# Kernel optimization log

Hardware: AMD Instinct MI355X
Metric: run time of the kernel (lower is better)

The kernel has to match this reference:

```python
import jax, jax.numpy as jnp
import numpy as np

N_PRED = 50000
N_GT = 2000


def _make_boxes(key, n, coord_scale=1000.0, wh_scale=100.0):
    k1, k2 = jax.random.split(key)
    xy = jax.random.uniform(k1, (n, 2), dtype=jnp.float32) * coord_scale
    wh = jax.random.uniform(k2, (n, 2), dtype=jnp.float32) * wh_scale + 1.0
    return jnp.concatenate([xy, xy + wh], axis=-1)  # xyxy


def setup_inputs() -> dict:
    key = jax.random.key(0)
    kp, kg = jax.random.split(key)
    return {
        "pred_bbox": _make_boxes(kp, N_PRED),
        "gt_bbox": _make_boxes(kg, N_GT),
    }


def _bbox_overlap(pred, gt):
    # pred: [N,4], gt: [M,4], xyxy -> IoU matrix [N,M]
    lt = jnp.maximum(pred[:, None, :2], gt[None, :, :2])  # [N,M,2]
    rb = jnp.minimum(pred[:, None, 2:], gt[None, :, 2:])  # [N,M,2]
    wh = jnp.clip(rb - lt, 0.0)
    inter = wh[..., 0] * wh[..., 1]  # [N,M]
    area_p = (pred[:, 2] - pred[:, 0]) * (pred[:, 3] - pred[:, 1])  # [N]
    area_g = (gt[:, 2] - gt[:, 0]) * (gt[:, 3] - gt[:, 1])  # [M]
    union = area_p[:, None] + area_g[None, :] - inter
    return inter / union


def reference(pred_bbox, gt_bbox):
    # OverlapCalculator.calc_overlap: detach pred, pairwise IoU, row-wise max
    iou = _bbox_overlap(jax.lax.stop_gradient(pred_bbox), gt_bbox)  # [N,M]
    max_overlap = jnp.max(iou, axis=1)          # [N]
    argmax_overlap = jnp.argmax(iou, axis=1)    # [N] int
    # forward returns (pred_bbox, gt_bbox, max, argmax) per image pair
    return (pred_bbox, gt_bbox, max_overlap, argmax_overlap)
```

## Files before the change

### kernel.cpp

```cpp
#include <hip/hip_runtime.h>


#define N_PRED 50000
#define N_GT   2000
#define NBIN   512
#define BLOCK  256
#define LPP    8
#define PPB    (BLOCK / LPP)

__device__ __forceinline__ int bin_of(float x, float xmin, float invw) {
    int b = (int)floorf((x - xmin) * invw);
    return max(0, min(NBIN - 1, b));
}

__global__ __launch_bounds__(512) void build_index(
        const float4* __restrict__ gt,
        float4* __restrict__ ws_gt, unsigned short* __restrict__ ws_idx,
        int* __restrict__ ws_bin, float* __restrict__ ws_par,
        float* __restrict__ out) {
#pragma clang fp contract(off)
    __shared__ float rmin[512], rmax[512], rw[512];
    __shared__ int   hist[NBIN], scan[NBIN], cursor[NBIN];
    __shared__ float s_par[3];
    const int tid = threadIdx.x;

    float mn = 3.4e38f, mx = -3.4e38f, mw = 0.0f;
    for (int j = tid; j < N_GT; j += 512) {
        const float4 g = gt[j];
        mn = fminf(mn, g.x);
        mx = fmaxf(mx, g.x);
        mw = fmaxf(mw, g.z - g.x);
        ((float4*)(out + 4 * N_PRED))[j] = g;
    }
    rmin[tid] = mn; rmax[tid] = mx; rw[tid] = mw;
    __syncthreads();
    for (int s = 256; s > 0; s >>= 1) {
        if (tid < s) {
            rmin[tid] = fminf(rmin[tid], rmin[tid + s]);
            rmax[tid] = fmaxf(rmax[tid], rmax[tid + s]);
            rw[tid]   = fmaxf(rw[tid],   rw[tid + s]);
        }
        __syncthreads();
    }
    if (tid == 0) {
        const float xmin  = rmin[0];
        const float range = fmaxf(rmax[0] - xmin, 1e-20f);
        s_par[0] = xmin;
        s_par[1] = (float)NBIN / range;
        s_par[2] = rw[0];
        ws_par[0] = s_par[0]; ws_par[1] = s_par[1]; ws_par[2] = s_par[2];
    }
    hist[tid] = 0;
    __syncthreads();
    const float xmin = s_par[0], invw = s_par[1];

    for (int j = tid; j < N_GT; j += 512)
        atomicAdd(&hist[bin_of(gt[j].x, xmin, invw)], 1);
    __syncthreads();

    const int v = hist[tid];
    scan[tid] = v;
    __syncthreads();
    for (int off = 1; off < NBIN; off <<= 1) {
        const int t = (tid >= off) ? scan[tid - off] : 0;
        __syncthreads();
        scan[tid] += t;
        __syncthreads();
    }
    const int excl = scan[tid] - v;
    cursor[tid] = excl;
    ws_bin[tid] = excl;
    if (tid == NBIN - 1) ws_bin[NBIN] = scan[tid];
    __syncthreads();

    for (int j = tid; j < N_GT; j += 512) {
        const float4 g = gt[j];
        const int pos = atomicAdd(&cursor[bin_of(g.x, xmin, invw)], 1);
        ws_gt[pos]  = g;
        ws_idx[pos] = (unsigned short)j;
    }
}

__global__ __launch_bounds__(BLOCK) void iou_max(
        const float4* __restrict__ pred,
        const float4* __restrict__ ws_gt, const unsigned short* __restrict__ ws_idx,
        const int* __restrict__ ws_bin, const float* __restrict__ ws_par,
        float* __restrict__ out) {
#pragma clang fp contract(off)
    __shared__ float4         sgt[N_GT];
    __shared__ unsigned short sidx[N_GT];
    __shared__ int            sbin[NBIN + 1];

    for (int j = threadIdx.x; j < N_GT; j += BLOCK) {
        sgt[j]  = ws_gt[j];
        sidx[j] = ws_idx[j];
    }
    for (int j = threadIdx.x; j < NBIN + 1; j += BLOCK) sbin[j] = ws_bin[j];
    const float xmin = ws_par[0], invw = ws_par[1], mgw = ws_par[2];
    __syncthreads();

    const int  pid = blockIdx.x * PPB + (int)(threadIdx.x >> 3);
    const int  sub = threadIdx.x & (LPP - 1);
    const bool act = pid < N_PRED;
    const float4 p  = pred[act ? pid : 0];
    const float  ap = (p.z - p.x) * (p.w - p.y);

    int lo = 0, hi = 0;
    if (act) {
        const int bl = bin_of(p.x - mgw - 0.5f, xmin, invw);
        const int bh = bin_of(p.z, xmin, invw);
        lo = sbin[bl];
        hi = sbin[bh + 1];
    }

    float best = 0.0f;
    int   bidx = 0;
    for (int t = lo + sub; t < hi; t += LPP) {
        const float4 g  = sgt[t];
        const int    oi = sidx[t];
        const float  ag = (g.z - g.x) * (g.w - g.y);
        const float  w  = fmaxf(fminf(p.z, g.z) - fmaxf(p.x, g.x), 0.0f);
        const float  h  = fmaxf(fminf(p.w, g.w) - fmaxf(p.y, g.y), 0.0f);
        const float  in = w * h;
        const float  un = (ap + ag) - in;
        const float  q  = in / un;
        if (q > best || (q == best && oi < bidx)) { best = q; bidx = oi; }
    }
#pragma unroll
    for (int s = 1; s < LPP; s <<= 1) {
        const float oq = __shfl_xor(best, s);
        const int   oi = __shfl_xor(bidx, s);
        if (oq > best || (oq == best && oi < bidx)) { best = oq; bidx = oi; }
    }
    if (act && sub == 0) {
        ((float4*)out)[pid] = p;
        out[4 * N_PRED + 4 * N_GT + pid]          = best;
        out[4 * N_PRED + 4 * N_GT + N_PRED + pid] = (float)bidx;
    }
}

extern "C" void kernel_launch(void* const* d_in, const int* in_sizes, int n_in,
                              void* d_out, int out_size, void* d_ws, size_t ws_size,
                              hipStream_t stream) {
    const float4* pred = (const float4*)d_in[0];
    const float4* gt   = (const float4*)d_in[1];
    float* out = (float*)d_out;

    char* ws = (char*)d_ws;
    float4*         ws_gt  = (float4*)ws;
    unsigned short* ws_idx = (unsigned short*)(ws + 32768);
    int*            ws_bin = (int*)(ws + 32768 + 4096);
    float*          ws_par = (float*)(ws + 32768 + 4096 + 2304);

    build_index<<<1, 512, 0, stream>>>(gt, ws_gt, ws_idx, ws_bin, ws_par, out);

    const int gx = (N_PRED + PPB - 1) / PPB;
    iou_max<<<gx, BLOCK, 0, stream>>>(pred, ws_gt, ws_idx, ws_bin, ws_par, out);
}
```

Before: 89.91 us.

## Replace 1D x-bin index with 2D x/y grid for GT candidate pruning

Builds a 32x16 spatial grid over ground-truth boxes (x-major, y-minor cells) instead of 512 x-only bins. Each prediction walks its x-bin range and, per x-bin, scans only the contiguous run of y-cells that could overlap, so far fewer non-overlapping GT boxes get an IoU evaluation. In exchange it adds a per-x-bin outer loop with two shared loads each, and the coarser x bins mean more per-column overhead and shorter inner loops for the 8 lanes to split.

```diff
diff --git a/kernel.cpp b/kernel.cpp
--- a/kernel.cpp
+++ b/kernel.cpp
@@ -3,65 +3,79 @@
 
 #define N_PRED 50000
 #define N_GT   2000
-#define NBIN   512
+#define NXB    32
+#define NYB    16
+#define NCELL  (NXB * NYB)
 #define BLOCK  256
 #define LPP    8
 #define PPB    (BLOCK / LPP)
 
-__device__ __forceinline__ int bin_of(float x, float xmin, float invw) {
-    int b = (int)floorf((x - xmin) * invw);
-    return max(0, min(NBIN - 1, b));
+__device__ __forceinline__ int bin1(float v, float mn, float inv, int nb) {
+    int b = (int)floorf((v - mn) * inv);
+    return max(0, min(nb - 1, b));
 }
 
 __global__ __launch_bounds__(512) void build_index(
         const float4* __restrict__ gt,
         float4* __restrict__ ws_gt, unsigned short* __restrict__ ws_idx,
-        int* __restrict__ ws_bin, float* __restrict__ ws_par,
+        int* __restrict__ ws_cell, float* __restrict__ ws_par,
         float* __restrict__ out) {
 #pragma clang fp contract(off)
-    __shared__ float rmin[512], rmax[512], rw[512];
-    __shared__ int   hist[NBIN], scan[NBIN], cursor[NBIN];
-    __shared__ float s_par[3];
+    __shared__ float rxm[512], rxM[512], rym[512], ryM[512], rw[512], rh[512];
+    __shared__ int   hist[NCELL], scan[NCELL], cursor[NCELL];
+    __shared__ float s_par[6];
     const int tid = threadIdx.x;
 
-    float mn = 3.4e38f, mx = -3.4e38f, mw = 0.0f;
+    float xm = 3.4e38f, xM = -3.4e38f, ym = 3.4e38f, yM = -3.4e38f;
+    float w = 0.0f, h = 0.0f;
     for (int j = tid; j < N_GT; j += 512) {
         const float4 g = gt[j];
-        mn = fminf(mn, g.x);
-        mx = fmaxf(mx, g.x);
-        mw = fmaxf(mw, g.z - g.x);
+        xm = fminf(xm, g.x); xM = fmaxf(xM, g.x);
+        ym = fminf(ym, g.y); yM = fmaxf(yM, g.y);
+        w  = fmaxf(w, g.z - g.x);
+        h  = fmaxf(h, g.w - g.y);
         ((float4*)(out + 4 * N_PRED))[j] = g;
     }
-    rmin[tid] = mn; rmax[tid] = mx; rw[tid] = mw;
+    rxm[tid] = xm; rxM[tid] = xM; rym[tid] = ym; ryM[tid] = yM;
+    rw[tid] = w;   rh[tid] = h;
     __syncthreads();
     for (int s = 256; s > 0; s >>= 1) {
         if (tid < s) {
-            rmin[tid] = fminf(rmin[tid], rmin[tid + s]);
-            rmax[tid] = fmaxf(rmax[tid], rmax[tid + s]);
-            rw[tid]   = fmaxf(rw[tid],   rw[tid + s]);
+            rxm[tid] = fminf(rxm[tid], rxm[tid + s]);
+            rxM[tid] = fmaxf(rxM[tid], rxM[tid + s]);
+            rym[tid] = fminf(rym[tid], rym[tid + s]);
+            ryM[tid] = fmaxf(ryM[tid], ryM[tid + s]);
+            rw[tid]  = fmaxf(rw[tid],  rw[tid + s]);
+            rh[tid]  = fmaxf(rh[tid],  rh[tid + s]);
         }
         __syncthreads();
     }
     if (tid == 0) {
-        const float xmin  = rmin[0];
-        const float range = fmaxf(rmax[0] - xmin, 1e-20f);
-        s_par[0] = xmin;
-        s_par[1] = (float)NBIN / range;
-        s_par[2] = rw[0];
-        ws_par[0] = s_par[0]; ws_par[1] = s_par[1]; ws_par[2] = s_par[2];
+        s_par[0] = rxm[0];
+        s_par[1] = (float)NXB / fmaxf(rxM[0] - rxm[0], 1e-20f);
+        s_par[2] = rym[0];
+        s_par[3] = (float)NYB / fmaxf(ryM[0] - rym[0], 1e-20f);
+        s_par[4] = rw[0];
+        s_par[5] = rh[0];
+        for (int k = 0; k < 6; ++k) ws_par[k] = s_par[k];
     }
     hist[tid] = 0;
     __syncthreads();
-    const float xmin = s_par[0], invw = s_par[1];
+    const float xmin = s_par[0], invx = s_par[1];
+    const float ymin = s_par[2], invy = s_par[3];
 
-    for (int j = tid; j < N_GT; j += 512)
-        atomicAdd(&hist[bin_of(gt[j].x, xmin, invw)], 1);
+    for (int j = tid; j < N_GT; j += 512) {
+        const float4 g = gt[j];
+        const int c = bin1(g.x, xmin, invx, NXB) * NYB +
+                      bin1(g.y, ymin, invy, NYB);
+        atomicAdd(&hist[c], 1);
+    }
     __syncthreads();
 
     const int v = hist[tid];
     scan[tid] = v;
     __syncthreads();
-    for (int off = 1; off < NBIN; off <<= 1) {
+    for (int off = 1; off < NCELL; off <<= 1) {
         const int t = (tid >= off) ? scan[tid - off] : 0;
         __syncthreads();
         scan[tid] += t;
@@ -69,13 +83,15 @@
     }
     const int excl = scan[tid] - v;
     cursor[tid] = excl;
-    ws_bin[tid] = excl;
-    if (tid == NBIN - 1) ws_bin[NBIN] = scan[tid];
+    ws_cell[tid] = excl;
+    if (tid == NCELL - 1) ws_cell[NCELL] = scan[tid];
     __syncthreads();
 
     for (int j = tid; j < N_GT; j += 512) {
         const float4 g = gt[j];
-        const int pos = atomicAdd(&cursor[bin_of(g.x, xmin, invw)], 1);
+        const int c = bin1(g.x, xmin, invx, NXB) * NYB +
+                      bin1(g.y, ymin, invy, NYB);
+        const int pos = atomicAdd(&cursor[c], 1);
         ws_gt[pos]  = g;
         ws_idx[pos] = (unsigned short)j;
     }
@@ -84,19 +100,21 @@
 __global__ __launch_bounds__(BLOCK) void iou_max(
         const float4* __restrict__ pred,
         const float4* __restrict__ ws_gt, const unsigned short* __restrict__ ws_idx,
-        const int* __restrict__ ws_bin, const float* __restrict__ ws_par,
+        const int* __restrict__ ws_cell, const float* __restrict__ ws_par,
         float* __restrict__ out) {
 #pragma clang fp contract(off)
     __shared__ float4         sgt[N_GT];
     __shared__ unsigned short sidx[N_GT];
-    __shared__ int            sbin[NBIN + 1];
+    __shared__ int            scell[NCELL + 1];
 
     for (int j = threadIdx.x; j < N_GT; j += BLOCK) {
         sgt[j]  = ws_gt[j];
         sidx[j] = ws_idx[j];
     }
-    for (int j = threadIdx.x; j < NBIN + 1; j += BLOCK) sbin[j] = ws_bin[j];
-    const float xmin = ws_par[0], invw = ws_par[1], mgw = ws_par[2];
+    for (int j = threadIdx.x; j < NCELL + 1; j += BLOCK) scell[j] = ws_cell[j];
+    const float xmin = ws_par[0], invx = ws_par[1];
+    const float ymin = ws_par[2], invy = ws_par[3];
+    const float mgw  = ws_par[4], mgh  = ws_par[5];
     __syncthreads();
 
     const int  pid = blockIdx.x * PPB + (int)(threadIdx.x >> 3);
@@ -105,26 +123,30 @@
     const float4 p  = pred[act ? pid : 0];
     const float  ap = (p.z - p.x) * (p.w - p.y);
 
-    int lo = 0, hi = 0;
+    int bl = 0, bh = -1, yl = 0, yh1 = 0;
     if (act) {
-        const int bl = bin_of(p.x - mgw - 0.5f, xmin, invw);
-        const int bh = bin_of(p.z, xmin, invw);
-        lo = sbin[bl];
-        hi = sbin[bh + 1];
+        bl  = bin1(p.x - mgw - 0.5f, xmin, invx, NXB);
+        bh  = bin1(p.z,              xmin, invx, NXB);
+        yl  = bin1(p.y - mgh - 0.5f, ymin, invy, NYB);
+        yh1 = bin1(p.w,              ymin, invy, NYB) + 1;
     }
 
     float best = 0.0f;
     int   bidx = 0;
-    for (int t = lo + sub; t < hi; t += LPP) {
-        const float4 g  = sgt[t];
-        const int    oi = sidx[t];
-        const float  ag = (g.z - g.x) * (g.w - g.y);
-        const float  w  = fmaxf(fminf(p.z, g.z) - fmaxf(p.x, g.x), 0.0f);
-        const float  h  = fmaxf(fminf(p.w, g.w) - fmaxf(p.y, g.y), 0.0f);
-        const float  in = w * h;
-        const float  un = (ap + ag) - in;
-        const float  q  = in / un;
-        if (q > best || (q == best && oi < bidx)) { best = q; bidx = oi; }
+    for (int b = bl; b <= bh; ++b) {
+        const int rlo = scell[b * NYB + yl];
+        const int rhi = scell[b * NYB + yh1];
+        for (int t = rlo + sub; t < rhi; t += LPP) {
+            const float4 g  = sgt[t];
+            const int    oi = sidx[t];
+            const float  ag = (g.z - g.x) * (g.w - g.y);
+            const float  w  = fmaxf(fminf(p.z, g.z) - fmaxf(p.x, g.x), 0.0f);
+            const float  h  = fmaxf(fminf(p.w, g.w) - fmaxf(p.y, g.y), 0.0f);
+            const float  in = w * h;
+            const float  un = (ap + ag) - in;
+            const float  q  = in / un;
+            if (q > best || (q == best && oi < bidx)) { best = q; bidx = oi; }
+        }
     }
 #pragma unroll
     for (int s = 1; s < LPP; s <<= 1) {
@@ -147,13 +169,13 @@
     float* out = (float*)d_out;
 
     char* ws = (char*)d_ws;
-    float4*         ws_gt  = (float4*)ws;
-    unsigned short* ws_idx = (unsigned short*)(ws + 32768);
-    int*            ws_bin = (int*)(ws + 32768 + 4096);
-    float*          ws_par = (float*)(ws + 32768 + 4096 + 2304);
+    float4*         ws_gt   = (float4*)ws;
+    unsigned short* ws_idx  = (unsigned short*)(ws + 32768);
+    int*            ws_cell = (int*)(ws + 32768 + 4096);
+    float*          ws_par  = (float*)(ws + 32768 + 4096 + 2304);
 
-    build_index<<<1, 512, 0, stream>>>(gt, ws_gt, ws_idx, ws_bin, ws_par, out);
+    build_index<<<1, 512, 0, stream>>>(gt, ws_gt, ws_idx, ws_cell, ws_par, out);
 
     const int gx = (N_PRED + PPB - 1) / PPB;
-    iou_max<<<gx, BLOCK, 0, stream>>>(pred, ws_gt, ws_idx, ws_bin, ws_par, out);
+    iou_max<<<gx, BLOCK, 0, stream>>>(pred, ws_gt, ws_idx, ws_cell, ws_par, out);
 }
```

Result: faster. 79.85 us (-11.2%).
